# Optimization experiments

Measured on AMD Instinct MI355X. Metric: run time of the kernel, lower is better.

The kernel has to match this reference:

```python
import jax, jax.numpy as jnp
import numpy as np

T, B = 50, 512
S, A, BEL, H, E, M = 256, 32, 1024, 1024, 1024, 256
MIN_STD = 0.1


def setup_inputs() -> dict:
    key = jax.random.key(0)
    ks = jax.random.split(key, 24)
    def rn(k, shape, scale=1.0):
        return jax.random.normal(k, shape, dtype=jnp.float32) * scale
    w = 0.05  # weight init scale
    return {
        "prev_state": rn(ks[0], (B, S)),
        "actions": rn(ks[1], (T, B, A)),
        "prev_belief": rn(ks[2], (B, BEL)),
        "observations": rn(ks[3], (T, B, E)),
        "nonterminals": jnp.ones((T, B, 1), dtype=jnp.float32),
        "map_embeddings": rn(ks[4], (T, B, M)),
        "map_embeddings_post": rn(ks[5], (T, B, M)),
        "noise_prior": rn(ks[6], (T, B, S)),
        "noise_post": rn(ks[7], (T, B, S)),
        "W_sa": rn(ks[8], (BEL, S + A + M), w), "b_sa": jnp.zeros((BEL,), jnp.float32),
        "W_ih": rn(ks[9], (3 * BEL, BEL), w), "b_ih": jnp.zeros((3 * BEL,), jnp.float32),
        "W_hh": rn(ks[10], (3 * BEL, BEL), w), "b_hh": jnp.zeros((3 * BEL,), jnp.float32),
        "W_bp": rn(ks[11], (H, BEL), w), "b_bp": jnp.zeros((H,), jnp.float32),
        "W_sp": rn(ks[12], (2 * S, H), w), "b_sp": jnp.zeros((2 * S,), jnp.float32),
        "W_bq": rn(ks[13], (H, BEL + E + M), w), "b_bq": jnp.zeros((H,), jnp.float32),
        "W_sq": rn(ks[14], (2 * S, H), w), "b_sq": jnp.zeros((2 * S,), jnp.float32),
    }


def reference(prev_state, actions, prev_belief, observations, nonterminals,
              map_embeddings, map_embeddings_post, noise_prior, noise_post,
              W_sa, b_sa, W_ih, b_ih, W_hh, b_hh,
              W_bp, b_bp, W_sp, b_sp, W_bq, b_bq, W_sq, b_sq):
    relu = jax.nn.relu
    def lin(x, W, b):
        return x @ W.T + b

    def gru(x, h):  # torch.nn.GRUCell math
        gi = x @ W_ih.T + b_ih
        gh = h @ W_hh.T + b_hh
        i_r, i_z, i_n = jnp.split(gi, 3, axis=1)
        h_r, h_z, h_n = jnp.split(gh, 3, axis=1)
        r = jax.nn.sigmoid(i_r + h_r)
        z = jax.nn.sigmoid(i_z + h_z)
        n = jnp.tanh(i_n + r * h_n)
        return (1.0 - z) * n + z * h

    def std(raw):
        return jnp.minimum(jax.nn.softplus(raw) + MIN_STD, 5.0)

    def step(carry, xs):
        belief, post_state = carry
        a, obs, nt, me, mp, np_, nq = xs
        s = post_state * nt
        hid = relu(lin(jnp.concatenate([s, a, me], axis=1), W_sa, b_sa))
        belief = gru(hid, belief)
        # prior p(z_t | h_t)
        hp = relu(lin(belief, W_bp, b_bp))
        p_mean, p_raw = jnp.split(lin(hp, W_sp, b_sp), 2, axis=1)
        p_std = std(p_raw)
        p_state = p_mean + p_std * np_
        # posterior q(z_t | h_t, e_t, m_t)
        hq = relu(lin(jnp.concatenate([belief, obs, mp], axis=1), W_bq, b_bq))
        q_mean, q_raw = jnp.split(lin(hq, W_sq, b_sq), 2, axis=1)
        q_std = std(q_raw)
        q_state = q_mean + q_std * nq
        return (belief, q_state), (belief, p_state, p_mean, p_std, q_state, q_mean, q_std)

    _, outs = jax.lax.scan(
        step, (prev_belief, prev_state),
        (actions, observations, nonterminals, map_embeddings,
         map_embeddings_post, noise_prior, noise_post))
    return outs  # 7 arrays, each (T, B, *)
```

## Files before the change

### kernel.cpp

```cpp
#include <hip/hip_runtime.h>
#include <hip/hip_bf16.h>

#define NT 50
#define NB 512
#define SD 256
#define AD 32
#define BD 1024
#define HD 1024
#define ED 1024
#define MD 256

typedef __attribute__((ext_vector_type(8))) short bf16x8;
typedef __attribute__((ext_vector_type(4))) float f32x4;

__device__ __forceinline__ void gload_lds16(const void* g, void* l) {
  __builtin_amdgcn_global_load_lds(
      (const __attribute__((address_space(1))) void*)g,
      (__attribute__((address_space(3))) void*)l, 16, 0, 0);
}

__device__ __forceinline__ float sigmoidf_(float x) { return 1.0f / (1.0f + __expf(-x)); }
__device__ __forceinline__ float softplusf_(float x) {
  return (x > 0.0f) ? (x + log1pf(__expf(-x))) : log1pf(__expf(x));
}

struct GDesc {
  const __hip_bfloat16* A1; const __hip_bfloat16* A2;
  int lda1, lda2, K1, K;
  const __hip_bfloat16* W; int ldw;
  const float* bias;
  float* Cf; __hip_bfloat16* Cb; int ldc;
};

template <int EPI>
__global__ __launch_bounds__(256) void gemm_bt(GDesc d0, GDesc d1) {
  const GDesc d = (blockIdx.z == 0) ? d0 : d1;
  __shared__ alignas(16) char lds[16384];

  const int tid = threadIdx.x;
  const int lane = tid & 63;
  const int w = tid >> 6;
  const int wr = w >> 1, wc = w & 1;
  const int m0 = blockIdx.x * 64;
  const int n0 = blockIdx.y * 64;

  f32x4 acc[2][2] = {};

  const __hip_bfloat16* a1row = d.A1 + (size_t)(m0 + lane) * d.lda1;
  const __hip_bfloat16* a2row = d.A2 ? d.A2 + (size_t)(m0 + lane) * d.lda2 : nullptr;
  const __hip_bfloat16* wrow = d.W + (size_t)(n0 + lane) * d.ldw;

  auto stage = [&](int buf, int k0) {
    char* la = lds + buf * 8192;
    char* lb = la + 4096;
    const __hip_bfloat16* as =
        (k0 < d.K1) ? (a1row + k0) : (a2row + (k0 - d.K1));
    gload_lds16(as + w * 8, la + w * 1024);
    gload_lds16(wrow + k0 + w * 8, lb + w * 1024);
  };

  stage(0, 0);
  int cur = 0;
  const int kc = lane >> 4, r15 = lane & 15;
  for (int k0 = 0;; k0 += 32) {
    __syncthreads();
    if (k0 + 32 < d.K) stage(cur ^ 1, k0 + 32);
    const char* la = lds + cur * 8192;
    const char* lb = la + 4096;
    bf16x8 af[2], bfr[2];
#pragma unroll
    for (int m = 0; m < 2; ++m)
      af[m] = *(const bf16x8*)(la + (size_t)(kc * 64 + wr * 32 + m * 16 + r15) * 16);
#pragma unroll
    for (int n = 0; n < 2; ++n)
      bfr[n] = *(const bf16x8*)(lb + (size_t)(kc * 64 + wc * 32 + n * 16 + r15) * 16);
#pragma unroll
    for (int m = 0; m < 2; ++m)
#pragma unroll
      for (int n = 0; n < 2; ++n)
        acc[m][n] = __builtin_amdgcn_mfma_f32_16x16x32_bf16(af[m], bfr[n], acc[m][n], 0, 0, 0);
    cur ^= 1;
    if (k0 + 32 >= d.K) break;
  }

  const int rg = lane >> 4;
#pragma unroll
  for (int m = 0; m < 2; ++m) {
#pragma unroll
    for (int n = 0; n < 2; ++n) {
      const int col = n0 + wc * 32 + n * 16 + r15;
      const float bv = d.bias[col];
#pragma unroll
      for (int i = 0; i < 4; ++i) {
        const int row = m0 + wr * 32 + m * 16 + rg * 4 + i;
        float v = acc[m][n][i] + bv;
        if (EPI == 1) {
          v = v > 0.0f ? v : 0.0f;
          d.Cb[(size_t)row * d.ldc + col] = __float2bfloat16(v);
        } else {
          d.Cf[(size_t)row * d.ldc + col] = v;
        }
      }
    }
  }
}

struct HDesc {
  const __hip_bfloat16* A; const __hip_bfloat16* W;
  const float* bias; const float* noise;
  float* st_o; float* mn_o; float* sd_o;
};

__global__ __launch_bounds__(256) void gemm_head(
    HDesc h0, HDesc h1, const float* __restrict__ ntn,
    __hip_bfloat16* __restrict__ sprev_b) {
  const HDesc h = (blockIdx.z == 0) ? h0 : h1;
  const bool isq = (blockIdx.z == 1);
  __shared__ alignas(16) char lds[16384];

  const int tid = threadIdx.x;
  const int lane = tid & 63;
  const int w = tid >> 6;
  const int wr = w >> 1, wc = w & 1;
  const int m0 = blockIdx.x * 64;
  const int n0 = blockIdx.y * 64;

  f32x4 acc[2][2] = {};
  const __hip_bfloat16* arow = h.A + (size_t)(m0 + lane) * HD;
  const __hip_bfloat16* wrow = h.W + (size_t)(n0 + lane) * HD;

  auto stage = [&](int buf, int k0) {
    char* la = lds + buf * 8192;
    gload_lds16(arow + k0 + w * 8, la + w * 1024);
    gload_lds16(wrow + k0 + w * 8, la + 4096 + w * 1024);
  };

  stage(0, 0);
  int cur = 0;
  const int kc = lane >> 4, r15 = lane & 15;
  for (int k0 = 0;; k0 += 32) {
    __syncthreads();
    if (k0 + 32 < HD) stage(cur ^ 1, k0 + 32);
    const char* la = lds + cur * 8192;
    const char* lb = la + 4096;
    bf16x8 af[2], bfr[2];
#pragma unroll
    for (int m = 0; m < 2; ++m)
      af[m] = *(const bf16x8*)(la + (size_t)(kc * 64 + wr * 32 + m * 16 + r15) * 16);
#pragma unroll
    for (int n = 0; n < 2; ++n)
      bfr[n] = *(const bf16x8*)(lb + (size_t)(kc * 64 + wc * 32 + n * 16 + r15) * 16);
#pragma unroll
    for (int m = 0; m < 2; ++m)
#pragma unroll
      for (int n = 0; n < 2; ++n)
        acc[m][n] = __builtin_amdgcn_mfma_f32_16x16x32_bf16(af[m], bfr[n], acc[m][n], 0, 0, 0);
    cur ^= 1;
    if (k0 + 32 >= HD) break;
  }

  const int rg = lane >> 4;
  const bool even = (r15 & 1) == 0;
#pragma unroll
  for (int m = 0; m < 2; ++m) {
#pragma unroll
    for (int n = 0; n < 2; ++n) {
      const int col = n0 + wc * 32 + n * 16 + r15;
      const int j = col >> 1;
      const float bv = h.bias[col];
#pragma unroll
      for (int i = 0; i < 4; ++i) {
        const int row = m0 + wr * 32 + m * 16 + rg * 4 + i;
        float v = acc[m][n][i] + bv;
        float partner = __shfl_xor(v, 1);
        float mean = even ? v : partner;
        float raw = even ? partner : v;
        float sd = fminf(softplusf_(raw) + 0.1f, 5.0f);
        const size_t o = (size_t)row * SD + j;
        if (even) {
          float st = mean + sd * h.noise[o];
          h.mn_o[o] = mean;
          h.st_o[o] = st;
          if (isq) sprev_b[o] = __float2bfloat16(st * ntn[row]);
        } else {
          h.sd_o[o] = sd;
        }
      }
    }
  }
}


__global__ void cvt_f32_bf16(const float* __restrict__ src, __hip_bfloat16* __restrict__ dst, int n) {
  int i = blockIdx.x * 256 + threadIdx.x;
  if (i < n) dst[i] = __float2bfloat16(src[i]);
}

__global__ void cvt_reorder_w(const float* __restrict__ src, __hip_bfloat16* __restrict__ dst) {
  int i = blockIdx.x * 256 + threadIdx.x;
  if (i >= 512 * 1024) return;
  int r = i >> 10, k = i & 1023;
  int dr = (r < 256) ? (2 * r) : (2 * (r - 256) + 1);
  dst[(size_t)dr * 1024 + k] = __float2bfloat16(src[i]);
}

__global__ void reorder_bias(const float* __restrict__ src, float* __restrict__ dst) {
  int i = blockIdx.x * 256 + threadIdx.x;
  if (i >= 512) return;
  int dr = (i < 256) ? (2 * i) : (2 * (i - 256) + 1);
  dst[dr] = src[i];
}

__global__ void build_actme(const float* __restrict__ act, const float* __restrict__ me,
                            __hip_bfloat16* __restrict__ dst) {
  int i = blockIdx.x * 256 + threadIdx.x;
  if (i >= NT * NB * 288) return;
  int tb = i / 288, j = i - tb * 288;
  float v = (j < AD) ? act[(size_t)tb * AD + j] : me[(size_t)tb * MD + (j - AD)];
  dst[i] = __float2bfloat16(v);
}

__global__ void init_state(const float* __restrict__ prev_state, const float* __restrict__ nt0,
                           const float* __restrict__ prev_belief,
                           __hip_bfloat16* __restrict__ sprev_b, __hip_bfloat16* __restrict__ bel_b) {
  int i = blockIdx.x * 256 + threadIdx.x;
  if (i >= NB * 1280) return;
  int b = i / 1280, j = i - b * 1280;
  if (j < SD) sprev_b[b * SD + j] = __float2bfloat16(prev_state[b * SD + j] * nt0[b]);
  else bel_b[(size_t)b * BD + (j - SD)] = __float2bfloat16(prev_belief[(size_t)b * BD + (j - SD)]);
}

__global__ void gru_obs(const float* __restrict__ gi, const float* __restrict__ gh,
                        const float* __restrict__ hprev,
                        const float* __restrict__ obs_t, const float* __restrict__ mp_t,
                        float* __restrict__ bel_out, __hip_bfloat16* __restrict__ bel_b,
                        __hip_bfloat16* __restrict__ obsmp_b) {
  int i = blockIdx.x * 256 + threadIdx.x;
  if (i >= NB * 2304) return;
  int b = i / 2304, j = i - b * 2304;
  if (j < BD) {
    const float* gib = gi + (size_t)b * 3072;
    const float* ghb = gh + (size_t)b * 3072;
    float r = sigmoidf_(gib[j] + ghb[j]);
    float z = sigmoidf_(gib[j + 1024] + ghb[j + 1024]);
    float n = tanhf(gib[j + 2048] + r * ghb[j + 2048]);
    float hv = hprev[(size_t)b * BD + j];
    float bel = (1.0f - z) * n + z * hv;
    bel_out[(size_t)b * BD + j] = bel;
    bel_b[(size_t)b * BD + j] = __float2bfloat16(bel);
  } else {
    int jj = j - BD;
    float v = (jj < ED) ? obs_t[(size_t)b * ED + jj] : mp_t[(size_t)b * MD + (jj - ED)];
    obsmp_b[(size_t)b * 1280 + jj] = __float2bfloat16(v);
  }
}


extern "C" void kernel_launch(void* const* d_in, const int* in_sizes, int n_in,
                              void* d_out, int out_size, void* d_ws, size_t ws_size,
                              hipStream_t stream) {
  const float* prev_state   = (const float*)d_in[0];
  const float* actions      = (const float*)d_in[1];
  const float* prev_belief  = (const float*)d_in[2];
  const float* observations = (const float*)d_in[3];
  const float* nonterminals = (const float*)d_in[4];
  const float* me           = (const float*)d_in[5];
  const float* mp           = (const float*)d_in[6];
  const float* noise_p      = (const float*)d_in[7];
  const float* noise_q      = (const float*)d_in[8];
  const float* W_sa = (const float*)d_in[9];  const float* b_sa = (const float*)d_in[10];
  const float* W_ih = (const float*)d_in[11]; const float* b_ih = (const float*)d_in[12];
  const float* W_hh = (const float*)d_in[13]; const float* b_hh = (const float*)d_in[14];
  const float* W_bp = (const float*)d_in[15]; const float* b_bp = (const float*)d_in[16];
  const float* W_sp = (const float*)d_in[17]; const float* b_sp = (const float*)d_in[18];
  const float* W_bq = (const float*)d_in[19]; const float* b_bq = (const float*)d_in[20];
  const float* W_sq = (const float*)d_in[21]; const float* b_sq = (const float*)d_in[22];
  float* out = (float*)d_out;

  char* p = (char*)d_ws;
  auto carve = [&](size_t bytes) -> char* {
    char* r = p;
    p += (bytes + 255) & ~(size_t)255;
    return r;
  };
  __hip_bfloat16* Wsa_b  = (__hip_bfloat16*)carve((size_t)BD * 544 * 2);
  __hip_bfloat16* Wih_b  = (__hip_bfloat16*)carve((size_t)3 * BD * BD * 2);
  __hip_bfloat16* Whh_b  = (__hip_bfloat16*)carve((size_t)3 * BD * BD * 2);
  __hip_bfloat16* Wbp_b  = (__hip_bfloat16*)carve((size_t)HD * BD * 2);
  __hip_bfloat16* Wsp_ro = (__hip_bfloat16*)carve((size_t)512 * HD * 2);
  __hip_bfloat16* Wbq_b  = (__hip_bfloat16*)carve((size_t)HD * 2304 * 2);
  __hip_bfloat16* Wsq_ro = (__hip_bfloat16*)carve((size_t)512 * HD * 2);
  float* bsp_ro = (float*)carve(512 * 4);
  float* bsq_ro = (float*)carve(512 * 4);
  __hip_bfloat16* actme_b = (__hip_bfloat16*)carve((size_t)NT * NB * 288 * 2);
  __hip_bfloat16* obsmp_b = (__hip_bfloat16*)carve((size_t)NB * 1280 * 2);
  __hip_bfloat16* sprev_b = (__hip_bfloat16*)carve((size_t)NB * SD * 2);
  __hip_bfloat16* bel_b   = (__hip_bfloat16*)carve((size_t)NB * BD * 2);
  __hip_bfloat16* hid_b   = (__hip_bfloat16*)carve((size_t)NB * BD * 2);
  __hip_bfloat16* hp_b    = (__hip_bfloat16*)carve((size_t)NB * HD * 2);
  __hip_bfloat16* hq_b    = (__hip_bfloat16*)carve((size_t)NB * HD * 2);
  float* gi_f = (float*)carve((size_t)NB * 3 * BD * 4);
  float* gh_f = (float*)carve((size_t)NB * 3 * BD * 4);

  auto cvt = [&](const float* s, __hip_bfloat16* d, int n) {
    cvt_f32_bf16<<<(n + 255) / 256, 256, 0, stream>>>(s, d, n);
  };
  cvt(W_sa, Wsa_b, BD * 544);
  cvt(W_ih, Wih_b, 3 * BD * BD);
  cvt(W_hh, Whh_b, 3 * BD * BD);
  cvt(W_bp, Wbp_b, HD * BD);
  cvt(W_bq, Wbq_b, HD * 2304);
  cvt_reorder_w<<<(512 * 1024 + 255) / 256, 256, 0, stream>>>(W_sp, Wsp_ro);
  cvt_reorder_w<<<(512 * 1024 + 255) / 256, 256, 0, stream>>>(W_sq, Wsq_ro);
  reorder_bias<<<2, 256, 0, stream>>>(b_sp, bsp_ro);
  reorder_bias<<<2, 256, 0, stream>>>(b_sq, bsq_ro);
  build_actme<<<(NT * NB * 288 + 255) / 256, 256, 0, stream>>>(actions, me, actme_b);
  init_state<<<(NB * 1280 + 255) / 256, 256, 0, stream>>>(prev_state, nonterminals,
                                                          prev_belief, sprev_b, bel_b);

  const size_t o_ps = (size_t)NT * NB * BD;
  const size_t blk  = (size_t)NT * NB * SD;

  for (int t = 0; t < NT; ++t) {
    const float* obs_t = observations + (size_t)t * NB * ED;
    const float* mp_t  = mp + (size_t)t * NB * MD;
    const float* np_t  = noise_p + (size_t)t * NB * SD;
    const float* nq_t  = noise_q + (size_t)t * NB * SD;
    float* out_bel = out + (size_t)t * NB * BD;
    const float* hprev = (t == 0) ? prev_belief : (out + (size_t)(t - 1) * NB * BD);
    const float* ntn = nonterminals + (size_t)((t + 1 < NT) ? t + 1 : t) * NB;

    {
      GDesc d{sprev_b, actme_b + (size_t)t * NB * 288, SD, 288, SD, 544,
              Wsa_b, 544, b_sa, nullptr, hid_b, BD};
      gemm_bt<1><<<dim3(8, 16, 1), 256, 0, stream>>>(d, d);
    }
    {
      GDesc di{hid_b, nullptr, BD, 0, BD, BD, Wih_b, BD, b_ih, gi_f, nullptr, 3 * BD};
      GDesc dh{bel_b, nullptr, BD, 0, BD, BD, Whh_b, BD, b_hh, gh_f, nullptr, 3 * BD};
      gemm_bt<0><<<dim3(8, 48, 2), 256, 0, stream>>>(di, dh);
    }
    gru_obs<<<(NB * 2304 + 255) / 256, 256, 0, stream>>>(gi_f, gh_f, hprev, obs_t, mp_t,
                                                         out_bel, bel_b, obsmp_b);
    {
      GDesc dp{bel_b, nullptr, BD, 0, BD, BD, Wbp_b, BD, b_bp, nullptr, hp_b, HD};
      GDesc dq{bel_b, obsmp_b, BD, 1280, BD, 2304, Wbq_b, 2304, b_bq, nullptr, hq_b, HD};
      gemm_bt<1><<<dim3(8, 16, 2), 256, 0, stream>>>(dp, dq);
    }
    {
      HDesc hp_{hp_b, Wsp_ro, bsp_ro, np_t,
                out + o_ps + (size_t)t * NB * SD,
                out + o_ps + blk + (size_t)t * NB * SD,
                out + o_ps + 2 * blk + (size_t)t * NB * SD};
      HDesc hq_{hq_b, Wsq_ro, bsq_ro, nq_t,
                out + o_ps + 3 * blk + (size_t)t * NB * SD,
                out + o_ps + 4 * blk + (size_t)t * NB * SD,
                out + o_ps + 5 * blk + (size_t)t * NB * SD};
      gemm_head<<<dim3(8, 8, 2), 256, 0, stream>>>(hp_, hq_, ntn, sprev_b);
    }
  }
}
```

Baseline: 5.694 ms.

## Unify GEMM kernels with 64x128 tiles, 4-stage LDS pipeline and swizzled block order

Replaces the separate GEMM and head kernels with a single templated kernel that computes 64x128 output tiles. K-chunks are loaded through a 4-deep ring of global-to-LDS buffers, synchronised with explicit vmcnt waits plus barriers, so several loads stay in flight during the MFMAs. Block indices are remapped so consecutive blocks share weight column panels, aiming for better L2 reuse. The larger tiles halve the block count per launch, which may leave many of the 256 CUs idle on these small grids, and the bigger LDS footprint can lower occupancy.

```diff
diff --git a/kernel.cpp b/kernel.cpp
--- a/kernel.cpp
+++ b/kernel.cpp
@@ -24,166 +24,136 @@
   return (x > 0.0f) ? (x + log1pf(__expf(-x))) : log1pf(__expf(x));
 }
 
-struct GDesc {
+struct GD {
   const __hip_bfloat16* A1; const __hip_bfloat16* A2;
   int lda1, lda2, K1, K;
   const __hip_bfloat16* W; int ldw;
   const float* bias;
   float* Cf; __hip_bfloat16* Cb; int ldc;
+  const float* noise; float* st_o; float* mn_o; float* sd_o;
+  const float* ntn; __hip_bfloat16* sprev; int isq;
 };
 
+#define WAITB(N)                                           \
+  asm volatile("s_waitcnt vmcnt(" #N ")" ::: "memory");    \
+  __builtin_amdgcn_s_barrier();                            \
+  __builtin_amdgcn_sched_barrier(0);
+
 template <int EPI>
-__global__ __launch_bounds__(256) void gemm_bt(GDesc d0, GDesc d1) {
-  const GDesc d = (blockIdx.z == 0) ? d0 : d1;
-  __shared__ alignas(16) char lds[16384];
+__global__ __launch_bounds__(256) void gemm_p(GD d0, GD d1) {
+  __shared__ alignas(16) char lds[4 * 12288];
+
+  const int NY = gridDim.y;
+  const int tot = NY * gridDim.z;
+  const int l = blockIdx.x + (blockIdx.y + blockIdx.z * NY) * 8;
+  const int ppx = tot >> 3;
+  const int q = l >> 3;
+  const int pan = (l & 7) * ppx + (q >> 3);
+  const int m0 = (q & 7) * 64;
+  const int n0 = (pan % NY) * 128;
+  const GD d = ((pan / NY) == 0) ? d0 : d1;
 
   const int tid = threadIdx.x;
   const int lane = tid & 63;
   const int w = tid >> 6;
   const int wr = w >> 1, wc = w & 1;
-  const int m0 = blockIdx.x * 64;
-  const int n0 = blockIdx.y * 64;
-
-  f32x4 acc[2][2] = {};
+
+  f32x4 acc[2][4] = {};
 
   const __hip_bfloat16* a1row = d.A1 + (size_t)(m0 + lane) * d.lda1;
   const __hip_bfloat16* a2row = d.A2 ? d.A2 + (size_t)(m0 + lane) * d.lda2 : nullptr;
-  const __hip_bfloat16* wrow = d.W + (size_t)(n0 + lane) * d.ldw;
+  const __hip_bfloat16* wrow0 = d.W + (size_t)(n0 + (w & 1) * 64 + lane) * d.ldw;
 
   auto stage = [&](int buf, int k0) {
-    char* la = lds + buf * 8192;
+    char* la = lds + (size_t)buf * 12288;
     char* lb = la + 4096;
-    const __hip_bfloat16* as =
-        (k0 < d.K1) ? (a1row + k0) : (a2row + (k0 - d.K1));
+    const __hip_bfloat16* as = (k0 < d.K1) ? (a1row + k0) : (a2row + (k0 - d.K1));
     gload_lds16(as + w * 8, la + w * 1024);
-    gload_lds16(wrow + k0 + w * 8, lb + w * 1024);
+    gload_lds16(wrow0 + k0 + (w >> 1) * 8, lb + w * 1024);
+    gload_lds16(wrow0 + k0 + (2 + (w >> 1)) * 8, lb + 4096 + w * 1024);
   };
 
-  stage(0, 0);
-  int cur = 0;
   const int kc = lane >> 4, r15 = lane & 15;
-  for (int k0 = 0;; k0 += 32) {
-    __syncthreads();
-    if (k0 + 32 < d.K) stage(cur ^ 1, k0 + 32);
-    const char* la = lds + cur * 8192;
+  auto compute = [&](int i) {
+    const char* la = lds + (size_t)(i & 3) * 12288;
     const char* lb = la + 4096;
-    bf16x8 af[2], bfr[2];
+    bf16x8 af[2], bfr[4];
 #pragma unroll
     for (int m = 0; m < 2; ++m)
       af[m] = *(const bf16x8*)(la + (size_t)(kc * 64 + wr * 32 + m * 16 + r15) * 16);
 #pragma unroll
-    for (int n = 0; n < 2; ++n)
-      bfr[n] = *(const bf16x8*)(lb + (size_t)(kc * 64 + wc * 32 + n * 16 + r15) * 16);
+    for (int n = 0; n < 4; ++n)
+      bfr[n] = *(const bf16x8*)(lb + (size_t)(kc * 128 + wc * 64 + n * 16 + r15) * 16);
 #pragma unroll
     for (int m = 0; m < 2; ++m)
 #pragma unroll
-      for (int n = 0; n < 2; ++n)
+      for (int n = 0; n < 4; ++n)
         acc[m][n] = __builtin_amdgcn_mfma_f32_16x16x32_bf16(af[m], bfr[n], acc[m][n], 0, 0, 0);
-    cur ^= 1;
-    if (k0 + 32 >= d.K) break;
+  };
+
+  const int n_it = d.K >> 5;
+  stage(0, 0);
+  stage(1, 32);
+  stage(2, 64);
+  int i = 0;
+  for (; i < n_it - 2; ++i) {
+    WAITB(6)
+    if (i < n_it - 3) stage((i + 3) & 3, (i + 3) << 5);
+    compute(i);
   }
+  WAITB(3)
+  compute(i);
+  ++i;
+  WAITB(0)
+  compute(i);
 
   const int rg = lane >> 4;
-#pragma unroll
-  for (int m = 0; m < 2; ++m) {
-#pragma unroll
-    for (int n = 0; n < 2; ++n) {
-      const int col = n0 + wc * 32 + n * 16 + r15;
-      const float bv = d.bias[col];
-#pragma unroll
-      for (int i = 0; i < 4; ++i) {
-        const int row = m0 + wr * 32 + m * 16 + rg * 4 + i;
-        float v = acc[m][n][i] + bv;
-        if (EPI == 1) {
-          v = v > 0.0f ? v : 0.0f;
-          d.Cb[(size_t)row * d.ldc + col] = __float2bfloat16(v);
-        } else {
-          d.Cf[(size_t)row * d.ldc + col] = v;
+  if (EPI == 2) {
+    const bool even = (r15 & 1) == 0;
+#pragma unroll
+    for (int m = 0; m < 2; ++m) {
+#pragma unroll
+      for (int n = 0; n < 4; ++n) {
+        const int col = n0 + wc * 64 + n * 16 + r15;
+        const int j = col >> 1;
+        const float bv = d.bias[col];
+#pragma unroll
+        for (int ii = 0; ii < 4; ++ii) {
+          const int row = m0 + wr * 32 + m * 16 + rg * 4 + ii;
+          float v = acc[m][n][ii] + bv;
+          float partner = __shfl_xor(v, 1);
+          float mean = even ? v : partner;
+          float raw = even ? partner : v;
+          float sd = fminf(softplusf_(raw) + 0.1f, 5.0f);
+          const size_t o = (size_t)row * SD + j;
+          if (even) {
+            float st = mean + sd * d.noise[o];
+            d.mn_o[o] = mean;
+            d.st_o[o] = st;
+            if (d.isq) d.sprev[o] = __float2bfloat16(st * d.ntn[row]);
+          } else {
+            d.sd_o[o] = sd;
+          }
         }
       }
     }
-  }
-}
-
-struct HDesc {
-  const __hip_bfloat16* A; const __hip_bfloat16* W;
-  const float* bias; const float* noise;
-  float* st_o; float* mn_o; float* sd_o;
-};
-
-__global__ __launch_bounds__(256) void gemm_head(
-    HDesc h0, HDesc h1, const float* __restrict__ ntn,
-    __hip_bfloat16* __restrict__ sprev_b) {
-  const HDesc h = (blockIdx.z == 0) ? h0 : h1;
-  const bool isq = (blockIdx.z == 1);
-  __shared__ alignas(16) char lds[16384];
-
-  const int tid = threadIdx.x;
-  const int lane = tid & 63;
-  const int w = tid >> 6;
-  const int wr = w >> 1, wc = w & 1;
-  const int m0 = blockIdx.x * 64;
-  const int n0 = blockIdx.y * 64;
-
-  f32x4 acc[2][2] = {};
-  const __hip_bfloat16* arow = h.A + (size_t)(m0 + lane) * HD;
-  const __hip_bfloat16* wrow = h.W + (size_t)(n0 + lane) * HD;
-
-  auto stage = [&](int buf, int k0) {
-    char* la = lds + buf * 8192;
-    gload_lds16(arow + k0 + w * 8, la + w * 1024);
-    gload_lds16(wrow + k0 + w * 8, la + 4096 + w * 1024);
-  };
-
-  stage(0, 0);
-  int cur = 0;
-  const int kc = lane >> 4, r15 = lane & 15;
-  for (int k0 = 0;; k0 += 32) {
-    __syncthreads();
-    if (k0 + 32 < HD) stage(cur ^ 1, k0 + 32);
-    const char* la = lds + cur * 8192;
-    const char* lb = la + 4096;
-    bf16x8 af[2], bfr[2];
-#pragma unroll
-    for (int m = 0; m < 2; ++m)
-      af[m] = *(const bf16x8*)(la + (size_t)(kc * 64 + wr * 32 + m * 16 + r15) * 16);
-#pragma unroll
-    for (int n = 0; n < 2; ++n)
-      bfr[n] = *(const bf16x8*)(lb + (size_t)(kc * 64 + wc * 32 + n * 16 + r15) * 16);
-#pragma unroll
-    for (int m = 0; m < 2; ++m)
-#pragma unroll
-      for (int n = 0; n < 2; ++n)
-        acc[m][n] = __builtin_amdgcn_mfma_f32_16x16x32_bf16(af[m], bfr[n], acc[m][n], 0, 0, 0);
-    cur ^= 1;
-    if (k0 + 32 >= HD) break;
-  }
-
-  const int rg = lane >> 4;
-  const bool even = (r15 & 1) == 0;
-#pragma unroll
-  for (int m = 0; m < 2; ++m) {
-#pragma unroll
-    for (int n = 0; n < 2; ++n) {
-      const int col = n0 + wc * 32 + n * 16 + r15;
-      const int j = col >> 1;
-      const float bv = h.bias[col];
-#pragma unroll
-      for (int i = 0; i < 4; ++i) {
-        const int row = m0 + wr * 32 + m * 16 + rg * 4 + i;
-        float v = acc[m][n][i] + bv;
-        float partner = __shfl_xor(v, 1);
-        float mean = even ? v : partner;
-        float raw = even ? partner : v;
-        float sd = fminf(softplusf_(raw) + 0.1f, 5.0f);
-        const size_t o = (size_t)row * SD + j;
-        if (even) {
-          float st = mean + sd * h.noise[o];
-          h.mn_o[o] = mean;
-          h.st_o[o] = st;
-          if (isq) sprev_b[o] = __float2bfloat16(st * ntn[row]);
-        } else {
-          h.sd_o[o] = sd;
+  } else {
+#pragma unroll
+    for (int m = 0; m < 2; ++m) {
+#pragma unroll
+      for (int n = 0; n < 4; ++n) {
+        const int col = n0 + wc * 64 + n * 16 + r15;
+        const float bv = d.bias[col];
+#pragma unroll
+        for (int ii = 0; ii < 4; ++ii) {
+          const int row = m0 + wr * 32 + m * 16 + rg * 4 + ii;
+          float v = acc[m][n][ii] + bv;
+          if (EPI == 1) {
+            v = v > 0.0f ? v : 0.0f;
+            d.Cb[(size_t)row * d.ldc + col] = __float2bfloat16(v);
+          } else {
+            d.Cf[(size_t)row * d.ldc + col] = v;
+          }
         }
       }
     }
@@ -321,6 +291,8 @@
   const size_t o_ps = (size_t)NT * NB * BD;
   const size_t blk  = (size_t)NT * NB * SD;
 
+  GD z{};
+
   for (int t = 0; t < NT; ++t) {
     const float* obs_t = observations + (size_t)t * NB * ED;
     const float* mp_t  = mp + (size_t)t * NB * MD;
@@ -331,32 +303,48 @@
     const float* ntn = nonterminals + (size_t)((t + 1 < NT) ? t + 1 : t) * NB;
 
     {
-      GDesc d{sprev_b, actme_b + (size_t)t * NB * 288, SD, 288, SD, 544,
-              Wsa_b, 544, b_sa, nullptr, hid_b, BD};
-      gemm_bt<1><<<dim3(8, 16, 1), 256, 0, stream>>>(d, d);
+      GD d = z;
+      d.A1 = sprev_b; d.lda1 = SD; d.K1 = SD;
+      d.A2 = actme_b + (size_t)t * NB * 288; d.lda2 = 288; d.K = 544;
+      d.W = Wsa_b; d.ldw = 544; d.bias = b_sa; d.Cb = hid_b; d.ldc = BD;
+      gemm_p<1><<<dim3(8, 8, 1), 256, 0, stream>>>(d, d);
     }
     {
-      GDesc di{hid_b, nullptr, BD, 0, BD, BD, Wih_b, BD, b_ih, gi_f, nullptr, 3 * BD};
-      GDesc dh{bel_b, nullptr, BD, 0, BD, BD, Whh_b, BD, b_hh, gh_f, nullptr, 3 * BD};
-      gemm_bt<0><<<dim3(8, 48, 2), 256, 0, stream>>>(di, dh);
+      GD di = z, dh = z;
+      di.A1 = hid_b; di.lda1 = BD; di.K1 = BD; di.K = BD;
+      di.W = Wih_b; di.ldw = BD; di.bias = b_ih; di.Cf = gi_f; di.ldc = 3 * BD;
+      dh.A1 = bel_b; dh.lda1 = BD; dh.K1 = BD; dh.K = BD;
+      dh.W = Whh_b; dh.ldw = BD; dh.bias = b_hh; dh.Cf = gh_f; dh.ldc = 3 * BD;
+      gemm_p<0><<<dim3(8, 24, 2), 256, 0, stream>>>(di, dh);
     }
     gru_obs<<<(NB * 2304 + 255) / 256, 256, 0, stream>>>(gi_f, gh_f, hprev, obs_t, mp_t,
                                                          out_bel, bel_b, obsmp_b);
     {
-      GDesc dp{bel_b, nullptr, BD, 0, BD, BD, Wbp_b, BD, b_bp, nullptr, hp_b, HD};
-      GDesc dq{bel_b, obsmp_b, BD, 1280, BD, 2304, Wbq_b, 2304, b_bq, nullptr, hq_b, HD};
-      gemm_bt<1><<<dim3(8, 16, 2), 256, 0, stream>>>(dp, dq);
+      GD dp = z, dq = z;
+      dp.A1 = bel_b; dp.lda1 = BD; dp.K1 = BD; dp.K = BD;
+      dp.W = Wbp_b; dp.ldw = BD; dp.bias = b_bp; dp.Cb = hp_b; dp.ldc = HD;
+      dq.A1 = bel_b; dq.lda1 = BD; dq.K1 = BD;
+      dq.A2 = obsmp_b; dq.lda2 = 1280; dq.K = 2304;
+      dq.W = Wbq_b; dq.ldw = 2304; dq.bias = b_bq; dq.Cb = hq_b; dq.ldc = HD;
+      gemm_p<1><<<dim3(8, 8, 2), 256, 0, stream>>>(dp, dq);
     }
     {
-      HDesc hp_{hp_b, Wsp_ro, bsp_ro, np_t,
-                out + o_ps + (size_t)t * NB * SD,
-                out + o_ps + blk + (size_t)t * NB * SD,
-                out + o_ps + 2 * blk + (size_t)t * NB * SD};
-      HDesc hq_{hq_b, Wsq_ro, bsq_ro, nq_t,
-                out + o_ps + 3 * blk + (size_t)t * NB * SD,
-                out + o_ps + 4 * blk + (size_t)t * NB * SD,
-                out + o_ps + 5 * blk + (size_t)t * NB * SD};
-      gemm_head<<<dim3(8, 8, 2), 256, 0, stream>>>(hp_, hq_, ntn, sprev_b);
+      GD hp_ = z, hq_ = z;
+      hp_.A1 = hp_b; hp_.lda1 = HD; hp_.K1 = HD; hp_.K = HD;
+      hp_.W = Wsp_ro; hp_.ldw = HD; hp_.bias = bsp_ro;
+      hp_.noise = np_t;
+      hp_.st_o = out + o_ps + (size_t)t * NB * SD;
+      hp_.mn_o = out + o_ps + blk + (size_t)t * NB * SD;
+      hp_.sd_o = out + o_ps + 2 * blk + (size_t)t * NB * SD;
+      hp_.ntn = ntn; hp_.sprev = sprev_b; hp_.isq = 0;
+      hq_.A1 = hq_b; hq_.lda1 = HD; hq_.K1 = HD; hq_.K = HD;
+      hq_.W = Wsq_ro; hq_.ldw = HD; hq_.bias = bsq_ro;
+      hq_.noise = nq_t;
+      hq_.st_o = out + o_ps + 3 * blk + (size_t)t * NB * SD;
+      hq_.mn_o = out + o_ps + 4 * blk + (size_t)t * NB * SD;
+      hq_.sd_o = out + o_ps + 5 * blk + (size_t)t * NB * SD;
+      hq_.ntn = ntn; hq_.sprev = sprev_b; hq_.isq = 1;
+      gemm_p<2><<<dim3(8, 4, 2), 256, 0, stream>>>(hp_, hq_);
     }
   }
 }
```

Result: slower. 5.929 ms (+4.1%).
